# Kernel tuning notes

Hardware: AMD Instinct MI355X
Metric: run time of the kernel (lower is better)

The kernel has to match this reference:

```python
import jax, jax.numpy as jnp
import numpy as np

B, H, W, DIM = 4, 128, 128, 64
HEADS, DH, DR = 8, 64, 16
INNER = HEADS * DH  # 512
HID3 = 3 * DR       # 48, wavelet-MLP in_channels
HIDX = 2 * HID3     # 96, wavelet-MLP hidden


def _conv(x, w, stride=1, pad=0, groups=1):
    return jax.lax.conv_general_dilated(
        x, w, (stride, stride), [(pad, pad), (pad, pad)],
        dimension_numbers=('NCHW', 'OIHW', 'NCHW'), feature_group_count=groups)


def _gelu(x):
    return jax.nn.gelu(x, approximate=False)  # torch nn.GELU default (erf)


def _haar_kernel(C):
    h = np.array([[1., 1.], [1., 1.]]) / 2.
    g = np.array([[1., -1.], [1., -1.]]) / 2.
    ht = np.array([[1., 1.], [-1., -1.]]) / 2.
    gt = np.array([[1., -1.], [-1., 1.]]) / 2.
    k = np.stack([h, g, ht, gt])[:, None]          # [4,1,2,2]
    return jnp.asarray(np.tile(k, (C, 1, 1, 1)), jnp.float32)  # [4C,1,2,2], torch repeat layout


def _l2norm(x):
    return x / jnp.maximum(jnp.linalg.norm(x, axis=-1, keepdims=True), 1e-12)


def _spatial(x, dw, pw, gamma):  # SpitialUnit, x NHWC
    t = x.transpose(0, 3, 1, 2)
    C = t.shape[1]
    y = _conv(t, dw, pad=1, groups=C)
    y = _conv(_gelu(y), pw)
    return (t + gamma * y).transpose(0, 2, 3, 1)


def _fourier(x, al_pw, al_dw, ah_pw, ah_dw, ph_pw, ph_scale):  # FourierUnit, x NHWC
    t = x.transpose(0, 3, 1, 2)
    Bc, C, Hc, Wc = t.shape
    X = jnp.fft.rfft2(t, norm='ortho')
    amp, phase = jnp.abs(X), jnp.angle(X)
    Hf, Wf = amp.shape[-2], amp.shape[-1]
    yy = jnp.linspace(0., 1., Hf)[:, None]
    xx = jnp.linspace(0., 1., Wf)[None, :]
    rr = jnp.sqrt(yy ** 2 + xx ** 2)
    low = jax.nn.sigmoid((0.25 - rr) * 20.0)
    high = 1.0 - low
    a_lo = _conv(_gelu(_conv(amp * low[None, None], al_pw)), al_dw, pad=1, groups=C)
    a_hi = _conv(_gelu(_conv(amp * high[None, None], ah_pw)), ah_dw, pad=1, groups=C)
    amp_out = a_lo + a_hi
    phase_out = phase + ph_scale * _conv(phase, ph_pw)
    Y = jax.lax.complex(amp_out * jnp.cos(phase_out), amp_out * jnp.sin(phase_out))
    out = jnp.fft.irfft2(Y, s=(Hc, Wc), norm='ortho')
    return out.transpose(0, 2, 3, 1)


def _wavelet(x, bn_gamma, bn_beta, mlp_in, mlp_dw, mlp_out, res_scale):  # WaveletUnit, x NHWC (H,W even)
    t = x.transpose(0, 3, 1, 2)
    Bc, C, Hc, Wc = t.shape
    y = _conv(t, _haar_kernel(C), stride=2, groups=C)           # [B,4C,H/2,W/2]
    LL, LH, HL, HH = jnp.split(y, 4, axis=1)                    # torch chunk layout
    high = jnp.concatenate([LH, HL, HH], axis=1)                # [B,3C,H/2,W/2]
    # BatchNorm2d in eval mode: running_mean=0, running_var=1, eps=1e-5
    n = high * (bn_gamma / jnp.sqrt(1.0 + 1e-5))[None, :, None, None] + bn_beta[None, :, None, None]
    m = _conv(n, mlp_in)
    m = _gelu(_conv(m, mlp_dw, pad=1, groups=m.shape[1]))
    m = _conv(m, mlp_out)
    high_enh = high + res_scale * m
    x1, x2, x3 = jnp.split(high_enh, 3, axis=1)
    # IWT: out[..., 2i+p, 2j+q] = [LL, x1; x2, x3][p,q]
    arr = jnp.stack([jnp.stack([LL, x1], -1), jnp.stack([x2, x3], -1)], axis=-2)  # [B,C,h,w,p,q]
    Hh, Wh = LL.shape[-2], LL.shape[-1]
    out = arr.transpose(0, 1, 2, 4, 3, 5).reshape(Bc, C, Hh * 2, Wh * 2)
    return out.transpose(0, 2, 3, 1)


def reference(x_in, Wq, Wk, Wv, Wr, We, qs_dw, qs_pw, qs_gamma,
              al_pw, al_dw, ah_pw, ah_dw, ph_pw, ph_scale,
              bn_gamma, bn_beta, mlp_in, mlp_dw, mlp_out, res_scale,
              rescale, Wproj, bproj):
    b, h, w, c = x_in.shape
    hw = h * w
    heads = rescale.shape[0]
    dh = Wq.shape[1] // heads
    dr = Wr.shape[1]
    x = x_in.reshape(b, hw, c)
    q_inp, k_inp, v_inp = x @ Wq, x @ Wk, x @ Wv
    q_dim = (q_inp @ Wr).reshape(b, h, w, dr)
    k_dim = (k_inp @ Wr).reshape(b, h, w, dr)
    v_dim = (v_inp @ Wr).reshape(b, h, w, dr)
    q_mix = _spatial(q_dim, qs_dw, qs_pw, qs_gamma)
    k_mix = _fourier(k_dim, al_pw, al_dw, ah_pw, ah_dw, ph_pw, ph_scale)
    v_mix = _wavelet(v_dim, bn_gamma, bn_beta, mlp_in, mlp_dw, mlp_out, res_scale)
    q_new = q_mix.reshape(b, hw, dr) @ We
    k_new = k_mix.reshape(b, hw, dr) @ We
    v_new = v_mix.reshape(b, hw, dr) @ We

    def pack(t):  # -> [b, heads, dh, hw]
        return t.reshape(b, hw, heads, dh).transpose(0, 2, 3, 1)

    q, k, v = pack(q_new), pack(k_new), pack(v_new)
    q, k = _l2norm(q), _l2norm(k)                       # normalize over hw
    attn = jnp.einsum('bhdn,bhen->bhde', k, q)          # channel attention [b,H,dh,dh]
    attn = jax.nn.softmax(attn * rescale[None], axis=-1)
    o = jnp.einsum('bhde,bhen->bhdn', attn, v)          # [b,H,dh,hw]
    o = o.transpose(0, 3, 1, 2).reshape(b, hw, heads * dh)
    return (o @ Wproj + bproj).reshape(b, h, w, c)


def setup_inputs() -> dict:
    key = jax.random.key(0)
    ks = jax.random.split(key, 20)

    def nrm(k, shape, s=0.02):
        return jax.random.normal(k, shape, jnp.float32) * s

    return {
        'x_in': jax.random.normal(ks[0], (B, H, W, DIM), jnp.float32),
        'Wq': nrm(ks[1], (DIM, INNER)), 'Wk': nrm(ks[2], (DIM, INNER)), 'Wv': nrm(ks[3], (DIM, INNER)),
        'Wr': nrm(ks[4], (INNER, DR)), 'We': nrm(ks[5], (DR, INNER)),
        'qs_dw': nrm(ks[6], (DR, 1, 3, 3)), 'qs_pw': nrm(ks[7], (DR, DR, 1, 1)),
        'qs_gamma': jnp.zeros((1, DR, 1, 1), jnp.float32),
        'al_pw': nrm(ks[8], (DR, DR, 1, 1)), 'al_dw': nrm(ks[9], (DR, 1, 3, 3)),
        'ah_pw': nrm(ks[10], (DR, DR, 1, 1)), 'ah_dw': nrm(ks[11], (DR, 1, 3, 3)),
        'ph_pw': nrm(ks[12], (DR, DR, 1, 1)), 'ph_scale': jnp.asarray(0.01, jnp.float32),
        'bn_gamma': jnp.ones((HID3,), jnp.float32), 'bn_beta': jnp.zeros((HID3,), jnp.float32),
        'mlp_in': nrm(ks[13], (HIDX, HID3, 1, 1)), 'mlp_dw': nrm(ks[14], (HIDX, 1, 3, 3)),
        'mlp_out': nrm(ks[15], (HID3, HIDX, 1, 1)), 'res_scale': jnp.ones((1,), jnp.float32),
        'rescale': jnp.ones((HEADS, 1, 1), jnp.float32),
        'Wproj': nrm(ks[16], (INNER, DIM)), 'bproj': jnp.zeros((DIM,), jnp.float32),
    }
```

## Files before the change

kernel.cpp:

```cpp
#include <hip/hip_runtime.h>
#include <hip/hip_bf16.h>
#include <math.h>

#define HW 16384

__device__ __forceinline__ float LD(const void* p, long i, int bf){
  return bf ? __bfloat162float(((const __hip_bfloat16*)p)[i]) : ((const float*)p)[i];
}
__device__ __forceinline__ float geluf(float x){ return 0.5f*x*(1.0f + erff(x*0.70710678118654752f)); }
__device__ __forceinline__ int rev7(int i){ return (int)(__brev((unsigned)i)>>25); }

__device__ __forceinline__ void fft128(float* Ar, float* Ai, const float* ct, const float* st,
                                       int lane, float dir){
  #pragma unroll
  for(int len=2; len<=128; len<<=1){
    int half=len>>1;
    int pos = lane & (half-1);
    int i1 = ((lane & ~(half-1))<<1) | pos;
    int i2 = i1 + half;
    int tw = pos * (128/len);
    float wr = ct[tw], wi = dir*st[tw];
    float xr=Ar[i2], xi=Ai[i2];
    float tr = xr*wr - xi*wi;
    float ti = xr*wi + xi*wr;
    float ur=Ar[i1], ui=Ai[i1];
    Ar[i1]=ur+tr; Ai[i1]=ui+ti;
    Ar[i2]=ur-tr; Ai[i2]=ui-ti;
  }
}

#define MAKE_TWP(ct,st) { int tt=threadIdx.x; if(tt<128){ float ang=6.283185307179586f*(float)tt/128.f; float s_,c_; sincosf(ang,&s_,&c_); (ct)[tt]=c_; (st)[tt]=s_; } }

#define OFF_M    0
#define OFF_G    3072
#define OFF_MB   6144
#define OFF_FLAG 10240
#define OFF_QDIM 16384
#define OFF_KDIM (16384 + 1048576)
#define OFF_VDIM (16384 + 2*1048576)
#define OFF_QMIX (16384 + 3*1048576)
#define OFF_KMIX (16384 + 4*1048576)
#define OFF_S    (16384 + 5*1048576)
#define FSZ 532480

__global__ void k_head(const void* Wq, const void* Wk, const void* Wv,
                       const void* Wr, const void* bng, float* ws){
  __shared__ float wr[8192];
  __shared__ float part[256];
  int blk=blockIdx.x, t=threadIdx.x;
  if(blk==48){
    for(int i=3072+t;i<10240;i+=256) ws[i]=0.f;
    if(t==0){
      float v = ((const float*)bng)[0];
      ((int*)ws)[OFF_FLAG] = (v==1.0f) ? 0 : 1;
    }
    return;
  }
  int bf = (((const float*)bng)[0]==1.0f) ? 0 : 1;
  int mat=blk>>4, seg=blk&15;
  const void* Wsrc = mat==0 ? Wq : (mat==1 ? Wk : Wv);
  for(int i=t;i<8192;i+=256) wr[i]=LD(Wr,i,bf);
  __syncthreads();
  int o=t&63, jseg=t>>6;
  int c=seg*4+(o>>4), r=o&15;
  float acc=0.f;
  for(int j=jseg*128;j<jseg*128+128;j++) acc += LD(Wsrc,(long)c*512+j,bf)*wr[j*16+r];
  part[jseg*64+o]=acc;
  __syncthreads();
  if(t<64){
    float s=part[t]+part[64+t]+part[128+t]+part[192+t];
    int cc=seg*4+(t>>4), rr=t&15;
    ws[mat*1024 + cc*16 + rr]=s;
  }
}

__global__ void k_dims(const void* x, const float* ws,
                       float* qd, float* kd, float* vd, const int* flg){
  int bf=*flg;
  __shared__ float xs[16*64];
  __shared__ float ms[3*1024];
  int b = blockIdx.x>>10;
  int pix0 = (blockIdx.x & 1023)<<4;
  int t = threadIdx.x;
  for(int i=t;i<3072;i+=256) ms[i]=ws[i];
  long base = ((long)b*HW + pix0)*64;
  for(int i=t;i<1024;i+=256) xs[i]=LD(x, base+i, bf);
  __syncthreads();
  int p=t>>4, r=t&15;
  float aq=0.f,ak=0.f,av=0.f;
  for(int c=0;c<64;c++){
    float xv = xs[p*64+c];
    aq += xv*ms[c*16+r];
    ak += xv*ms[1024+c*16+r];
    av += xv*ms[2048+c*16+r];
  }
  long o = ((long)b*HW + pix0)*16 + t;
  qd[o]=aq; kd[o]=ak; vd[o]=av;
}

__global__ void k_mix3(const float* qd, float* qm, const void* dw, const void* pw, const void* gamma,
                       const float* kd, float* Rre, float* Rim,
                       const float* vd, float* m96, const void* win, const void* bng, const void* bnb,
                       const int* flg){
  __shared__ float smem[9664];
  int bf=*flg;
  int blk=blockIdx.x, t=threadIdx.x;
  if(blk<256){
    float* tile=smem; float* dws=smem+8704; float* pws=smem+8848; float* gsm=smem+9104;
    int b=blk>>6, y0=(blk&63)<<1;
    for(int i=t;i<144;i+=256) dws[i]=LD(dw,i,bf);
    if(t<256) pws[t]=LD(pw,t,bf);
    if(t<16) gsm[t]=LD(gamma,t,bf);
    for(int i=t;i<8192;i+=256){
      int ry=i>>11, rem=i&2047, xx=rem>>4, ch=rem&15;
      int yy=y0-1+ry;
      tile[(ry*128+xx)*17+ch] = (yy>=0&&yy<128) ? qd[(long)(b*128+yy)*2048 + rem] : 0.f;
    }
    __syncthreads();
    int ty=t>>7, x=t&127;
    float g[16];
    for(int ch=0;ch<16;ch++){
      float acc=0.f;
      for(int p=0;p<3;p++)
        for(int q=0;q<3;q++){
          int xx=x-1+q;
          if(xx>=0&&xx<128) acc += dws[ch*9+p*3+q]*tile[((ty+p)*128+xx)*17+ch];
        }
      g[ch]=geluf(acc);
    }
    long ob = ((long)(b*128+y0+ty)*128 + x)*16;
    for(int c=0;c<16;c++){
      float acc=0.f;
      for(int ch=0;ch<16;ch++) acc += pws[c*16+ch]*g[ch];
      qm[ob+c] = tile[((1+ty)*128+x)*17+c] + gsm[c]*acc;
    }
  } else if(blk<512){
    float* slab=smem; float* outre=smem+4160; float* outim=smem+6272;
    float* Ar=smem+8384; float* Ai=smem+8896; float* ct=smem+9408; float* st=smem+9536;
    int blk2=blk-256;
    int b=blk2>>6, y0=(blk2&63)<<1;
    MAKE_TWP(ct,st);
    long gbase = ((long)(b*128+y0))*2048;
    for(int e=t;e<4096;e+=256){
      int yl=e>>11, rem=e&2047, x=rem>>4, c=rem&15;
      slab[yl*2080 + c*130 + x] = kd[gbase + e];
    }
    __syncthreads();
    int w=t>>6, l=t&63, wb=w<<7;
    for(int li=w; li<32; li+=4){
      int yl=li>>4, c=li&15;
      int sb = yl*2080 + c*130;
      float v0=slab[sb+l], v1=slab[sb+64+l];
      int r0=rev7(l), r1=rev7(64+l);
      Ar[wb+r0]=v0; Ai[wb+r0]=0.f;
      Ar[wb+r1]=v1; Ai[wb+r1]=0.f;
      fft128(Ar+wb, Ai+wb, ct, st, l, -1.f);
      int ob = yl*1056 + c*66;
      outre[ob+l]=Ar[wb+l]; outim[ob+l]=Ai[wb+l];
      if(l==0){ outre[ob+64]=Ar[wb+64]; outim[ob+64]=Ai[wb+64]; }
    }
    __syncthreads();
    long obase = ((long)(b*128+y0))*1040;
    for(int e=t;e<2080;e+=256){
      int yl=e/1040, rem=e%1040, v=rem>>4, c=rem&15;
      Rre[obase+e]=outre[yl*1056 + c*66 + v];
      Rim[obase+e]=outim[yl*1056 + c*66 + v];
    }
  } else {
    float* wi=smem; float* vds=smem+4608; float* ns=smem+5632;
    float* gsm=smem+6400; float* bsm=smem+6448;
    int blk3=blk-512;
    int b = blk3>>8;
    int ij0 = (blk3&255)<<4;
    for(int i=t;i<4608;i+=256){ int cc=i/96, ch=i%96; wi[cc*96+ch]=LD(win,(long)ch*48+cc,bf); }
    if(t<48){ gsm[t]=LD(bng,t,bf)*(1.f/sqrtf(1.f+1e-5f)); bsm[t]=LD(bnb,t,bf); }
    int i0 = ij0>>6, j0 = ij0&63;
    long rb0 = ((long)(b*128 + 2*i0)*128 + 2*j0)*16;
    for(int i=t;i<512;i+=256){ vds[i]=vd[rb0+i]; vds[512+i]=vd[rb0+2048+i]; }
    __syncthreads();
    for(int o=t;o<768;o+=256){
      int p=o/48, cc2=o%48;
      int m=cc2+16, c=m>>2, f=m&3;
      float a =vds[(2*p)*16+c],     bv=vds[(2*p+1)*16+c];
      float cv=vds[512+(2*p)*16+c], dv=vds[512+(2*p+1)*16+c];
      float v;
      if(f==0)      v=(a+bv+cv+dv);
      else if(f==1) v=(a-bv+cv-dv);
      else if(f==2) v=(a+bv-cv-dv);
      else          v=(a-bv-cv+dv);
      ns[o] = v*0.5f*gsm[cc2]+bsm[cc2];
    }
    __syncthreads();
    long ob = ((long)b*4096 + ij0)*96;
    for(int o=t;o<1536;o+=256){
      int p=o/96, ch=o%96;
      float acc=0.f;
      for(int cc=0;cc<48;cc++) acc += wi[cc*96+ch]*ns[p*48+cc];
      m96[ob+o]=acc;
    }
  }
}

__global__ void k_fft_col(const float* Rre, const float* Rim,
                          float* glo, float* ghi, float* pho,
                          const void* alpw, const void* ahpw,
                          const void* phpw, const void* phs, const int* flg){
  __shared__ float sre[2080], sim[2080];
  __shared__ float og[2080], oh[2080], op[2080];
  __shared__ float Ar[512], Ai[512];
  __shared__ float ct[128], st[128];
  __shared__ float wl[256], wh[256], wp[256];
  int t=threadIdx.x;
  int bf=*flg;
  int b = blockIdx.x/65, v = blockIdx.x%65;
  MAKE_TWP(ct,st);
  wl[t]=LD(alpw,t,bf); wh[t]=LD(ahpw,t,bf); wp[t]=LD(phpw,t,bf);
  long ibase = ((long)b*128)*1040 + v*16;
  for(int e=t;e<2048;e+=256){
    int y=e>>4, c=e&15;
    sre[c*130+y]=Rre[ibase + (long)y*1040 + c];
    sim[c*130+y]=Rim[ibase + (long)y*1040 + c];
  }
  __syncthreads();
  int w=t>>6, l=t&63, wb=w<<7;
  const float inv=1.f/128.f;
  for(int c=w; c<16; c+=4){
    int sb=c*130;
    float x0r=sre[sb+l], x0i=sim[sb+l], x1r=sre[sb+64+l], x1i=sim[sb+64+l];
    int r0=rev7(l), r1=rev7(64+l);
    Ar[wb+r0]=x0r; Ai[wb+r0]=x0i;
    Ar[wb+r1]=x1r; Ai[wb+r1]=x1i;
    fft128(Ar+wb, Ai+wb, ct, st, l, -1.f);
    float re0=Ar[wb+l]*inv, im0=Ai[wb+l]*inv;
    float re1=Ar[wb+64+l]*inv, im1=Ai[wb+64+l]*inv;
    sre[sb+l]=sqrtf(re0*re0+im0*im0); sim[sb+l]=atan2f(im0,re0);
    sre[sb+64+l]=sqrtf(re1*re1+im1*im1); sim[sb+64+l]=atan2f(im1,re1);
  }
  __syncthreads();
  {
    int u = t&127, half = t>>7;
    float yy=(float)u/127.f, xx=(float)v/64.f;
    float rr=sqrtf(yy*yy+xx*xx);
    float lo = 1.f/(1.f+expf((rr-0.25f)*20.f));
    float hi = 1.f-lo;
    float av[16], pv[16];
    for(int ch=0;ch<16;ch++){ av[ch]=sre[ch*130+u]; pv[ch]=sim[ch*130+u]; }
    float pscale = LD(phs,0,bf);
    for(int c=half*8;c<half*8+8;c++){
      float al=0.f, ah=0.f, pp=0.f;
      for(int ch=0;ch<16;ch++){
        float a=av[ch];
        al += wl[c*16+ch]*(a*lo);
        ah += wh[c*16+ch]*(a*hi);
        pp += wp[c*16+ch]*pv[ch];
      }
      og[c*130+u]=geluf(al); oh[c*130+u]=geluf(ah); op[c*130+u]=pv[c]+pscale*pp;
    }
  }
  __syncthreads();
  long obase = ((long)b*128)*1040 + v*16;
  for(int e=t;e<2048;e+=256){
    int u=e>>4, c=e&15;
    long o = obase + (long)u*1040 + c;
    glo[o]=og[c*130+u]; ghi[o]=oh[c*130+u]; pho[o]=op[c*130+u];
  }
}

__global__ void k_four_dw(const float* glo, const float* ghi, const float* pho,
                          float* Yre, float* Yim,
                          const void* aldw, const void* ahdw, const int* flg){
  int bf=*flg;
  __shared__ float wl[144], wh[144];
  int t=threadIdx.x;
  if(t<144){wl[t]=LD(aldw,t,bf); wh[t]=LD(ahdw,t,bf);}
  __syncthreads();
  long o = (long)blockIdx.x*256+t;
  int c=(int)(o&15); long r=o>>4; int v=(int)(r%65); long r2=r/65; int u=(int)(r2&127); int b=(int)(r2>>7);
  float acc=0.f;
  for(int dp=0;dp<3;dp++){
    int uu=u-1+dp; if(uu<0||uu>=128) continue;
    for(int dq=0;dq<3;dq++){
      int vv=v-1+dq; if(vv<0||vv>=65) continue;
      long idx=(((long)(b*128+uu))*65+vv)*16+c;
      acc += wl[c*9+dp*3+dq]*glo[idx] + wh[c*9+dp*3+dq]*ghi[idx];
    }
  }
  float pvv = pho[o];
  float s_,c_; sincosf(pvv,&s_,&c_);
  Yre[o]=acc*c_; Yim[o]=acc*s_;
}

__global__ void k_ifft_col(const float* Yre, const float* Yim, float* Zre, float* Zim){
  __shared__ float sre[2080], sim[2080];
  __shared__ float Ar[512], Ai[512];
  __shared__ float ct[128], st[128];
  int t=threadIdx.x;
  int b = blockIdx.x/65, v = blockIdx.x%65;
  MAKE_TWP(ct,st);
  long ibase = ((long)b*128)*1040 + v*16;
  for(int e=t;e<2048;e+=256){
    int u=e>>4, c=e&15;
    sre[c*130+u]=Yre[ibase + (long)u*1040 + c];
    sim[c*130+u]=Yim[ibase + (long)u*1040 + c];
  }
  __syncthreads();
  int w=t>>6, l=t&63, wb=w<<7;
  for(int c=w; c<16; c+=4){
    int sb=c*130;
    float x0r=sre[sb+l], x0i=sim[sb+l], x1r=sre[sb+64+l], x1i=sim[sb+64+l];
    int r0=rev7(l), r1=rev7(64+l);
    Ar[wb+r0]=x0r; Ai[wb+r0]=x0i;
    Ar[wb+r1]=x1r; Ai[wb+r1]=x1i;
    fft128(Ar+wb, Ai+wb, ct, st, l, +1.f);
    sre[sb+l]=Ar[wb+l]; sim[sb+l]=Ai[wb+l];
    sre[sb+64+l]=Ar[wb+64+l]; sim[sb+64+l]=Ai[wb+64+l];
  }
  __syncthreads();
  for(int e=t;e<2048;e+=256){
    int y=e>>4, c=e&15;
    Zre[ibase + (long)y*1040 + c]=sre[c*130+y];
    Zim[ibase + (long)y*1040 + c]=sim[c*130+y];
  }
}

__global__ void k_mix2(const float* Zre, const float* Zim, float* km,
                       const float* m96, float* g96, const void* wdw_, const int* flg){
  __shared__ float smem[9664];
  int blk=blockIdx.x, t=threadIdx.x;
  if(blk<256){
    float* szre=smem; float* szim=smem+2112; float* oslab=smem+4224;
    float* Ar=smem+8384; float* Ai=smem+8896; float* ct=smem+9408; float* st=smem+9536;
    int b = blk>>6, y0 = (blk&63)<<1;
    MAKE_TWP(ct,st);
    long ibase = ((long)(b*128+y0))*1040;
    for(int e=t;e<2080;e+=256){
      int yl=e/1040, rem=e%1040, v=rem>>4, c=rem&15;
      szre[yl*1056 + c*66 + v]=Zre[ibase+e];
      szim[yl*1056 + c*66 + v]=Zim[ibase+e];
    }
    __syncthreads();
    int w=t>>6, l=t&63, wb=w<<7;
    const float inv=1.f/128.f;
    for(int li=w; li<32; li+=4){
      int yl=li>>4, c=li&15;
      int sb = yl*1056 + c*66;
      float zr0 = szre[sb+l];
      float zi0 = (l==0)?0.f:szim[sb+l];
      float zr1, zi1;
      if(l==0){ zr1=szre[sb+64]; zi1=0.f; }
      else    { zr1=szre[sb+64-l]; zi1=-szim[sb+64-l]; }
      int r0=rev7(l), r1=rev7(64+l);
      Ar[wb+r0]=zr0; Ai[wb+r0]=zi0;
      Ar[wb+r1]=zr1; Ai[wb+r1]=zi1;
      fft128(Ar+wb, Ai+wb, ct, st, l, +1.f);
      int ob = yl*2080 + c*130;
      oslab[ob+l]=Ar[wb+l]*inv;
      oslab[ob+64+l]=Ar[wb+64+l]*inv;
    }
    __syncthreads();
    long obase = ((long)(b*128+y0))*2048;
    for(int e=t;e<4096;e+=256){
      int yl=e>>11, rem=e&2047, x=rem>>4, c=rem&15;
      km[obase+e]=oslab[yl*2080 + c*130 + x];
    }
  } else {
    int bf=*flg;
    float* wdw=smem;
    for(int i=t;i<864;i+=256) wdw[i]=LD(wdw_,i,bf);
    __syncthreads();
    int o = (blk-256)*256+t;
    int ch = o%96; int r = o/96; int px = r&4095; int b = r>>12;
    int i = px>>6, j = px&63;
    long mb = (long)b*393216;
    float acc=0.f;
    for(int dp=0;dp<3;dp++){ int ii=i-1+dp; if(ii<0||ii>=64) continue;
      for(int dq=0;dq<3;dq++){ int jj=j-1+dq; if(jj<0||jj>=64) continue;
        acc += wdw[ch*9+dp*3+dq]*m96[mb + (long)(ii*64+jj)*96 + ch]; } }
    g96[o]=geluf(acc);
  }
}

__global__ void k_gram(const float* qm, const float* km, float* G){
  __shared__ float qs[256*16], ks[256*16];
  int b=blockIdx.x>>5; int chunk=blockIdx.x&31;
  int t=threadIdx.x; int r=t>>4, s=t&15;
  float akq=0.f, akk=0.f, aqq=0.f;
  for(int tile=0;tile<2;tile++){
    long pb=((long)b*HW + chunk*512 + tile*256)*16;
    for(int i=t;i<4096;i+=256){ qs[i]=qm[pb+i]; ks[i]=km[pb+i]; }
    __syncthreads();
    for(int p=0;p<256;p++){
      float kv=ks[p*16+r], qv=qs[p*16+s];
      akq += kv*qv;
      akk += kv*ks[p*16+s];
      aqq += qs[p*16+r]*qv;
    }
    __syncthreads();
  }
  float* Gb=G + b*768;
  atomicAdd(&Gb[t], akq);
  atomicAdd(&Gb[256+t], akk);
  atomicAdd(&Gb[512+t], aqq);
}

__global__ void k_attn(const float* G, float* Mb, const void* We,
                       const void* Wproj, const void* resc, const int* flg){
  int bf=*flg;
  __shared__ float wes[16*64];
  __shared__ float gkq[256], gkk[256], gqq[256];
  __shared__ float ukq[64*16], ukk[64*16], uqq[64*16];
  __shared__ float nk[64], nq[64];
  __shared__ float A[64*64];
  __shared__ float T[64*16];
  __shared__ float wpj[64*64];
  int b=blockIdx.x>>3, h=blockIdx.x&7;
  int t=threadIdx.x;
  for(int i=t;i<1024;i+=256){ int rr=i>>6, e=i&63; wes[rr*64+e]=LD(We, (long)rr*512 + h*64 + e, bf); }
  gkq[t]=G[b*768+t]; gkk[t]=G[b*768+256+t]; gqq[t]=G[b*768+512+t];
  for(int i=t;i<4096;i+=256){ int d=i>>6, c=i&63; wpj[i]=LD(Wproj,(long)(h*64+d)*64+c,bf); }
  __syncthreads();
  for(int i=t;i<1024;i+=256){
    int d=i>>4, s=i&15;
    float a1=0.f,a2=0.f,a3=0.f;
    for(int rr=0;rr<16;rr++){ float wv=wes[rr*64+d]; a1+=wv*gkq[rr*16+s]; a2+=wv*gkk[rr*16+s]; a3+=wv*gqq[rr*16+s]; }
    ukq[i]=a1; ukk[i]=a2; uqq[i]=a3;
  }
  __syncthreads();
  if(t<64){ float a=0.f; for(int s=0;s<16;s++) a+=ukk[t*16+s]*wes[s*64+t]; nk[t]=fmaxf(sqrtf(a),1e-12f); }
  else if(t<128){ int e=t-64; float a=0.f; for(int s=0;s<16;s++) a+=uqq[e*16+s]*wes[s*64+e]; nq[e]=fmaxf(sqrtf(a),1e-12f); }
  __syncthreads();
  float rsc=LD(resc,h,bf);
  for(int i=t;i<4096;i+=256){
    int d=i>>6, e=i&63;
    float a=0.f; for(int s=0;s<16;s++) a+=ukq[d*16+s]*wes[s*64+e];
    A[i]=a/(nk[d]*nq[e])*rsc;
  }
  __syncthreads();
  if(t<64){
    int d=t; float m=-1e30f;
    for(int e=0;e<64;e++) m=fmaxf(m,A[d*64+e]);
    float sum=0.f;
    for(int e=0;e<64;e++){ float ev=expf(A[d*64+e]-m); A[d*64+e]=ev; sum+=ev; }
    float inv=1.f/sum;
    for(int e=0;e<64;e++) A[d*64+e]*=inv;
  }
  __syncthreads();
  for(int i=t;i<1024;i+=256){
    int d=i>>4, s=i&15;
    float a=0.f; for(int e=0;e<64;e++) a+=A[d*64+e]*wes[s*64+e];
    T[i]=a;
  }
  __syncthreads();
  for(int i=t;i<1024;i+=256){
    int s=i>>6, c=i&63;
    float a=0.f; for(int d=0;d<64;d++) a+=T[d*16+s]*wpj[d*64+c];
    atomicAdd(&Mb[b*1024 + s*64 + c], a);
  }
}

__global__ void k_epi2(const float* g96, const float* vd, const float* Mb_,
                       const void* wout_, const void* rs_, const void* bproj,
                       void* out, const int* flg){
  int bf=*flg;
  __shared__ __align__(16) float sg[32*104];
  __shared__ __align__(16) float swt[48*100];
  __shared__ __align__(16) float smb[1024];
  __shared__ float sbias[64];
  int t=threadIdx.x;
  int b = blockIdx.x>>7;
  int rem = blockIdx.x&127;
  int gi = rem>>1;
  int gj0 = (rem&1)<<5;

  long gb = ((long)b*4096 + gi*64 + gj0)*96;
  for(int e=t;e<3072;e+=256){ int px=e/96, ch=e-px*96; sg[px*104+ch]=g96[gb+e]; }
  for(int e=t;e<4608;e+=256){ int cc=e/96, ch=e-cc*96; swt[cc*100+ch]=LD(wout_, e, bf); }
  for(int i=t;i<1024;i+=256) smb[i]=Mb_[b*1024+i];
  if(t<64) sbias[t]=LD(bproj,t,bf);
  __syncthreads();

  int tpx=t>>4, tcc=t&15;
  int px0=tpx<<1, cc0=tcc*3;
  float a00=0.f,a01=0.f,a02=0.f,a10=0.f,a11=0.f,a12=0.f;
  const float4* g4=(const float4*)sg;
  const float4* w4=(const float4*)swt;
  #pragma unroll 4
  for(int ch4=0; ch4<24; ch4++){
    float4 ga=g4[px0*26+ch4], gbv=g4[(px0+1)*26+ch4];
    float4 w0=w4[cc0*25+ch4], w1=w4[(cc0+1)*25+ch4], w2=w4[(cc0+2)*25+ch4];
    a00 += ga.x*w0.x+ga.y*w0.y+ga.z*w0.z+ga.w*w0.w;
    a01 += ga.x*w1.x+ga.y*w1.y+ga.z*w1.z+ga.w*w1.w;
    a02 += ga.x*w2.x+ga.y*w2.y+ga.z*w2.z+ga.w*w2.w;
    a10 += gbv.x*w0.x+gbv.y*w0.y+gbv.z*w0.z+gbv.w*w0.w;
    a11 += gbv.x*w1.x+gbv.y*w1.y+gbv.z*w1.z+gbv.w*w1.w;
    a12 += gbv.x*w2.x+gbv.y*w2.y+gbv.z*w2.z+gbv.w*w2.w;
  }
  __syncthreads();

  float* she = sg;
  float rs=LD(rs_,0,bf);
  float accv[2][3]={{a00,a01,a02},{a10,a11,a12}};
  #pragma unroll
  for(int i=0;i<2;i++)
    #pragma unroll
    for(int j=0;j<3;j++){
      int pxl=px0+i, cc=cc0+j, gj=gj0+pxl;
      int m=cc+16, c=m>>2, f=m&3;
      long vb=((long)(b*128+2*gi)*128 + 2*gj)*16;
      float a=vd[vb+c], bv=vd[vb+16+c], cv=vd[vb+2048+c], dv=vd[vb+2064+c];
      float hv;
      if(f==0)      hv=(a+bv+cv+dv);
      else if(f==1) hv=(a-bv+cv-dv);
      else if(f==2) hv=(a+bv-cv-dv);
      else          hv=(a-bv-cv+dv);
      she[pxl*64 + 16 + cc] = hv*0.5f + rs*accv[i][j];
    }
  for(int o=t;o<512;o+=256){
    int pxl=o>>4, c16=o&15, gj=gj0+pxl;
    int c=c16>>2, f=c16&3;
    long vb=((long)(b*128+2*gi)*128 + 2*gj)*16;
    float a=vd[vb+c], bv=vd[vb+16+c], cv=vd[vb+2048+c], dv=vd[vb+2064+c];
    float hv;
    if(f==0)      hv=(a+bv+cv+dv);
    else if(f==1) hv=(a-bv+cv-dv);
    else if(f==2) hv=(a+bv-cv-dv);
    else          hv=(a-bv-cv+dv);
    she[pxl*64 + c16] = hv*0.5f;
  }
  __syncthreads();

  int c=t&63, xg=t>>6;
  float mbr[16];
  #pragma unroll
  for(int s=0;s<16;s++) mbr[s]=smb[s*64+c];
  float bb=sbias[c];
  long ob0 = ((long)(b*128+2*gi)*128 + 2*gj0)*64;
  for(int k=0;k<32;k++){
    int o=xg+(k<<2);
    int r=o>>6, xl=o&63;
    int hp=xl>>1, pos=((r&1)<<1)|(xl&1);
    const float4* h4=(const float4*)(she + hp*64 + pos*16);
    float4 h0=h4[0],h1=h4[1],h2=h4[2],h3=h4[3];
    float acc=bb;
    acc += h0.x*mbr[0]+h0.y*mbr[1]+h0.z*mbr[2]+h0.w*mbr[3];
    acc += h1.x*mbr[4]+h1.y*mbr[5]+h1.z*mbr[6]+h1.w*mbr[7];
    acc += h2.x*mbr[8]+h2.y*mbr[9]+h2.z*mbr[10]+h2.w*mbr[11];
    acc += h3.x*mbr[12]+h3.y*mbr[13]+h3.z*mbr[14]+h3.w*mbr[15];
    long oo = ob0 + (long)r*8192 + (long)xl*64 + c;
    if(bf) ((__hip_bfloat16*)out)[oo]=__float2bfloat16(acc);
    else   ((float*)out)[oo]=acc;
  }
}

extern "C" void kernel_launch(void* const* d_in, const int* in_sizes, int n_in,
                              void* d_out, int out_size, void* d_ws, size_t ws_size,
                              hipStream_t stream) {
  const void* x_in   = d_in[0];
  const void* Wq     = d_in[1];
  const void* Wk     = d_in[2];
  const void* Wv     = d_in[3];
  const void* Wr     = d_in[4];
  const void* We     = d_in[5];
  const void* qs_dw  = d_in[6];
  const void* qs_pw  = d_in[7];
  const void* qs_g   = d_in[8];
  const void* al_pw  = d_in[9];
  const void* al_dw  = d_in[10];
  const void* ah_pw  = d_in[11];
  const void* ah_dw  = d_in[12];
  const void* ph_pw  = d_in[13];
  const void* ph_s   = d_in[14];
  const void* bn_g   = d_in[15];
  const void* bn_b   = d_in[16];
  const void* mlp_in = d_in[17];
  const void* mlp_dw = d_in[18];
  const void* mlp_out= d_in[19];
  const void* res_s  = d_in[20];
  const void* rescale= d_in[21];
  const void* Wproj  = d_in[22];
  const void* bproj  = d_in[23];
  float* ws = (float*)d_ws;
  const int* flg = ((const int*)ws) + OFF_FLAG;

  float* FA = ws + OFF_S;
  float* FB = FA + FSZ;
  float* FC = FB + FSZ;
  float* FD = FC + FSZ;
  float* FE = FD + FSZ;
  float* M96 = FE + FSZ;
  float* G96 = ws + OFF_QDIM;

  k_head<<<49,256,0,stream>>>(Wq,Wk,Wv,Wr,bn_g, ws);
  k_dims<<<4096,256,0,stream>>>(x_in, ws, ws+OFF_QDIM, ws+OFF_KDIM, ws+OFF_VDIM, flg);
  k_mix3<<<1536,256,0,stream>>>(ws+OFF_QDIM, ws+OFF_QMIX, qs_dw, qs_pw, qs_g,
                                ws+OFF_KDIM, FA, FB,
                                ws+OFF_VDIM, M96, mlp_in, bn_g, bn_b, flg);
  k_fft_col<<<260,256,0,stream>>>(FA, FB, FC, FD, FE, al_pw, ah_pw, ph_pw, ph_s, flg);
  k_four_dw<<<2080,256,0,stream>>>(FC, FD, FE, FA, FB, al_dw, ah_dw, flg);
  k_ifft_col<<<260,256,0,stream>>>(FA, FB, FC, FD);
  k_mix2<<<6400,256,0,stream>>>(FC, FD, ws+OFF_KMIX, M96, G96, mlp_dw, flg);
  k_gram<<<128,256,0,stream>>>(ws+OFF_QMIX, ws+OFF_KMIX, ws+OFF_G);
  k_attn<<<32,256,0,stream>>>(ws+OFF_G, ws+OFF_MB, We, Wproj, rescale, flg);
  k_epi2<<<512,256,0,stream>>>(G96, ws+OFF_VDIM, ws+OFF_MB, mlp_out, res_s, bproj, d_out, flg);
}
```

Before: 295.6 us.

## Register-tile dims and wavelet-MLP projections, prepack weights, split gram blocks

```diff
diff --git a/kernel.cpp b/kernel.cpp
--- a/kernel.cpp
+++ b/kernel.cpp
@@ -35,6 +35,9 @@
 #define OFF_G    3072
 #define OFF_MB   6144
 #define OFF_FLAG 10240
+#define OFF_WIN  10752
+#define OFF_GSM  15360
+#define OFF_BSM  15408
 #define OFF_QDIM 16384
 #define OFF_KDIM (16384 + 1048576)
 #define OFF_VDIM (16384 + 2*1048576)
@@ -44,12 +47,19 @@
 #define FSZ 532480
 
 __global__ void k_head(const void* Wq, const void* Wk, const void* Wv,
-                       const void* Wr, const void* bng, float* ws){
+                       const void* Wr, const void* bng, const void* bnb,
+                       const void* mlp_in_, float* ws){
   __shared__ float wr[8192];
   __shared__ float part[256];
   int blk=blockIdx.x, t=threadIdx.x;
   if(blk==48){
+    int bf = (((const float*)bng)[0]==1.0f) ? 0 : 1;
     for(int i=3072+t;i<10240;i+=256) ws[i]=0.f;
+    for(int i=t;i<4608;i+=256) ws[OFF_WIN+i]=LD(mlp_in_, i, bf);
+    if(t<48){
+      ws[OFF_GSM+t]=LD(bng,t,bf)*(1.f/sqrtf(1.f+1e-5f));
+      ws[OFF_BSM+t]=LD(bnb,t,bf);
+    }
     if(t==0){
       float v = ((const float*)bng)[0];
       ((int*)ws)[OFF_FLAG] = (v==1.0f) ? 0 : 1;
@@ -70,39 +80,70 @@
   if(t<64){
     float s=part[t]+part[64+t]+part[128+t]+part[192+t];
     int cc=seg*4+(t>>4), rr=t&15;
-    ws[mat*1024 + cc*16 + rr]=s;
+    ws[(mat*16+rr)*64 + cc]=s;
   }
 }
 
 __global__ void k_dims(const void* x, const float* ws,
                        float* qd, float* kd, float* vd, const int* flg){
   int bf=*flg;
-  __shared__ float xs[16*64];
-  __shared__ float ms[3*1024];
-  int b = blockIdx.x>>10;
-  int pix0 = (blockIdx.x & 1023)<<4;
-  int t = threadIdx.x;
-  for(int i=t;i<3072;i+=256) ms[i]=ws[i];
-  long base = ((long)b*HW + pix0)*64;
-  for(int i=t;i<1024;i+=256) xs[i]=LD(x, base+i, bf);
-  __syncthreads();
-  int p=t>>4, r=t&15;
-  float aq=0.f,ak=0.f,av=0.f;
-  for(int c=0;c<64;c++){
-    float xv = xs[p*64+c];
-    aq += xv*ms[c*16+r];
-    ak += xv*ms[1024+c*16+r];
-    av += xv*ms[2048+c*16+r];
-  }
-  long o = ((long)b*HW + pix0)*16 + t;
-  qd[o]=aq; kd[o]=ak; vd[o]=av;
+  __shared__ float sh[128*49];
+  int t=threadIdx.x;
+  int b = blockIdx.x>>7;
+  int pix0 = (blockIdx.x&127)<<7;
+  int w=t>>6, l=t&63;
+  int pxl = ((w&1)<<6) + l;
+  int rh = w>>1;
+  long base = ((long)b*HW + pix0 + pxl)*64;
+
+  float xr[64];
+  if(!bf){
+    const float4* xp = (const float4*)((const float*)x + base);
+    #pragma unroll
+    for(int k=0;k<16;k++){
+      float4 v = xp[k];
+      xr[4*k]=v.x; xr[4*k+1]=v.y; xr[4*k+2]=v.z; xr[4*k+3]=v.w;
+    }
+  } else {
+    const uint4* xp = (const uint4*)((const __hip_bfloat16*)x + base);
+    #pragma unroll
+    for(int k=0;k<8;k++){
+      uint4 u = xp[k];
+      unsigned uu[4]={u.x,u.y,u.z,u.w};
+      #pragma unroll
+      for(int q=0;q<4;q++){
+        xr[8*k+2*q]   = __uint_as_float((uu[q]&0xffffu)<<16);
+        xr[8*k+2*q+1] = __uint_as_float(uu[q]&0xffff0000u);
+      }
+    }
+  }
+  for(int r=rh*24; r<rh*24+24; r++){
+    const float* mrow = ws + r*64;
+    float a0=0.f,a1=0.f,a2=0.f,a3=0.f;
+    #pragma unroll
+    for(int c=0;c<64;c+=4){
+      a0 += xr[c]  *mrow[c];
+      a1 += xr[c+1]*mrow[c+1];
+      a2 += xr[c+2]*mrow[c+2];
+      a3 += xr[c+3]*mrow[c+3];
+    }
+    sh[pxl*49 + r] = (a0+a1)+(a2+a3);
+  }
+  __syncthreads();
+  long ob = ((long)b*HW + pix0)*16;
+  for(int e=t;e<2048;e+=256){
+    int px=e>>4, rr=e&15;
+    qd[ob+e]=sh[px*49 + rr];
+    kd[ob+e]=sh[px*49 + 16 + rr];
+    vd[ob+e]=sh[px*49 + 32 + rr];
+  }
 }
 
 __global__ void k_mix3(const float* qd, float* qm, const void* dw, const void* pw, const void* gamma,
                        const float* kd, float* Rre, float* Rim,
-                       const float* vd, float* m96, const void* win, const void* bng, const void* bnb,
+                       const float* vd, float* m96, const float* wsb,
                        const int* flg){
-  __shared__ float smem[9664];
+  __shared__ float smem[12416];
   int bf=*flg;
   int blk=blockIdx.x, t=threadIdx.x;
   if(blk<256){
@@ -167,36 +208,61 @@
       Rim[obase+e]=outim[yl*1056 + c*66 + v];
     }
   } else {
-    float* wi=smem; float* vds=smem+4608; float* ns=smem+5632;
-    float* gsm=smem+6400; float* bsm=smem+6448;
-    int blk3=blk-512;
-    int b = blk3>>8;
-    int ij0 = (blk3&255)<<4;
-    for(int i=t;i<4608;i+=256){ int cc=i/96, ch=i%96; wi[cc*96+ch]=LD(win,(long)ch*48+cc,bf); }
-    if(t<48){ gsm[t]=LD(bng,t,bf)*(1.f/sqrtf(1.f+1e-5f)); bsm[t]=LD(bnb,t,bf); }
-    int i0 = ij0>>6, j0 = ij0&63;
-    long rb0 = ((long)(b*128 + 2*i0)*128 + 2*j0)*16;
-    for(int i=t;i<512;i+=256){ vds[i]=vd[rb0+i]; vds[512+i]=vd[rb0+2048+i]; }
+    float* sm=smem;
+    const float* winf = wsb + OFF_WIN;
+    const float* gsmf = wsb + OFF_GSM;
+    const float* bsmf = wsb + OFF_BSM;
+    int idx3 = blk-512;
+    int b = idx3>>5;
+    int hpbase = (idx3&31)<<7;
+    int w=t>>6, l=t&63;
+    int hpl = ((w>>1)<<6) + l;
+    int chh = w&1;
+    int hp = hpbase + hpl;
+    int i = hp>>6, j = hp&63;
+    float va[4][12];
+    #pragma unroll
+    for(int pi=0;pi<2;pi++)
+      #pragma unroll
+      for(int pj=0;pj<2;pj++){
+        long vb = ((long)(b*128 + 2*i+pi)*128 + (2*j+pj))*16 + 4;
+        const float4* vp=(const float4*)(vd+vb);
+        float4 v0=vp[0], v1=vp[1], v2=vp[2];
+        float* d=va[pi*2+pj];
+        d[0]=v0.x;d[1]=v0.y;d[2]=v0.z;d[3]=v0.w;
+        d[4]=v1.x;d[5]=v1.y;d[6]=v1.z;d[7]=v1.w;
+        d[8]=v2.x;d[9]=v2.y;d[10]=v2.z;d[11]=v2.w;
+      }
+    float ns[48];
+    #pragma unroll
+    for(int cc=0;cc<48;cc++){
+      int m=cc+16, c=(m>>2)-4, f=m&3;
+      float a=va[0][c], bv=va[1][c], cv=va[2][c], dvv=va[3][c];
+      float v;
+      if(f==0)      v=(a+bv+cv+dvv);
+      else if(f==1) v=(a-bv+cv-dvv);
+      else if(f==2) v=(a+bv-cv-dvv);
+      else          v=(a-bv-cv+dvv);
+      ns[cc]=v*0.5f*gsmf[cc]+bsmf[cc];
+    }
+    for(int k=0;k<48;k++){
+      int ch = chh*48 + k;
+      const float* wrow = winf + ch*48;
+      float a0=0.f,a1=0.f,a2=0.f,a3=0.f;
+      #pragma unroll
+      for(int cc=0;cc<48;cc+=4){
+        a0 += ns[cc]  *wrow[cc];
+        a1 += ns[cc+1]*wrow[cc+1];
+        a2 += ns[cc+2]*wrow[cc+2];
+        a3 += ns[cc+3]*wrow[cc+3];
+      }
+      sm[ch*129 + hpl] = (a0+a1)+(a2+a3);
+    }
     __syncthreads();
-    for(int o=t;o<768;o+=256){
-      int p=o/48, cc2=o%48;
-      int m=cc2+16, c=m>>2, f=m&3;
-      float a =vds[(2*p)*16+c],     bv=vds[(2*p+1)*16+c];
-      float cv=vds[512+(2*p)*16+c], dv=vds[512+(2*p+1)*16+c];
-      float v;
-      if(f==0)      v=(a+bv+cv+dv);
-      else if(f==1) v=(a-bv+cv-dv);
-      else if(f==2) v=(a+bv-cv-dv);
-      else          v=(a-bv-cv+dv);
-      ns[o] = v*0.5f*gsm[cc2]+bsm[cc2];
-    }
-    __syncthreads();
-    long ob = ((long)b*4096 + ij0)*96;
-    for(int o=t;o<1536;o+=256){
-      int p=o/96, ch=o%96;
-      float acc=0.f;
-      for(int cc=0;cc<48;cc++) acc += wi[cc*96+ch]*ns[p*48+cc];
-      m96[ob+o]=acc;
+    long ob = ((long)b*4096 + hpbase)*96;
+    for(int e=t;e<12288;e+=256){
+      int hpp=e/96, ch=e-hpp*96;
+      m96[ob+e]=sm[ch*129 + hpp];
     }
   }
 }
@@ -382,20 +448,17 @@
 
 __global__ void k_gram(const float* qm, const float* km, float* G){
   __shared__ float qs[256*16], ks[256*16];
-  int b=blockIdx.x>>5; int chunk=blockIdx.x&31;
+  int b=blockIdx.x>>6; int chunk=blockIdx.x&63;
   int t=threadIdx.x; int r=t>>4, s=t&15;
+  long pb=((long)b*HW + chunk*256)*16;
+  for(int i=t;i<4096;i+=256){ qs[i]=qm[pb+i]; ks[i]=km[pb+i]; }
+  __syncthreads();
   float akq=0.f, akk=0.f, aqq=0.f;
-  for(int tile=0;tile<2;tile++){
-    long pb=((long)b*HW + chunk*512 + tile*256)*16;
-    for(int i=t;i<4096;i+=256){ qs[i]=qm[pb+i]; ks[i]=km[pb+i]; }
-    __syncthreads();
-    for(int p=0;p<256;p++){
-      float kv=ks[p*16+r], qv=qs[p*16+s];
-      akq += kv*qv;
-      akk += kv*ks[p*16+s];
-      aqq += qs[p*16+r]*qv;
-    }
-    __syncthreads();
+  for(int p=0;p<256;p++){
+    float kv=ks[p*16+r], qv=qs[p*16+s];
+    akq += kv*qv;
+    akk += kv*ks[p*16+s];
+    aqq += qs[p*16+r]*qv;
   }
   float* Gb=G + b*768;
   atomicAdd(&Gb[t], akq);
@@ -590,16 +653,16 @@
   float* M96 = FE + FSZ;
   float* G96 = ws + OFF_QDIM;
 
-  k_head<<<49,256,0,stream>>>(Wq,Wk,Wv,Wr,bn_g, ws);
-  k_dims<<<4096,256,0,stream>>>(x_in, ws, ws+OFF_QDIM, ws+OFF_KDIM, ws+OFF_VDIM, flg);
-  k_mix3<<<1536,256,0,stream>>>(ws+OFF_QDIM, ws+OFF_QMIX, qs_dw, qs_pw, qs_g,
-                                ws+OFF_KDIM, FA, FB,
-                                ws+OFF_VDIM, M96, mlp_in, bn_g, bn_b, flg);
+  k_head<<<49,256,0,stream>>>(Wq,Wk,Wv,Wr,bn_g,bn_b,mlp_in, ws);
+  k_dims<<<512,256,0,stream>>>(x_in, ws, ws+OFF_QDIM, ws+OFF_KDIM, ws+OFF_VDIM, flg);
+  k_mix3<<<640,256,0,stream>>>(ws+OFF_QDIM, ws+OFF_QMIX, qs_dw, qs_pw, qs_g,
+                               ws+OFF_KDIM, FA, FB,
+                               ws+OFF_VDIM, M96, ws, flg);
   k_fft_col<<<260,256,0,stream>>>(FA, FB, FC, FD, FE, al_pw, ah_pw, ph_pw, ph_s, flg);
   k_four_dw<<<2080,256,0,stream>>>(FC, FD, FE, FA, FB, al_dw, ah_dw, flg);
   k_ifft_col<<<260,256,0,stream>>>(FA, FB, FC, FD);
   k_mix2<<<6400,256,0,stream>>>(FC, FD, ws+OFF_KMIX, M96, G96, mlp_dw, flg);
-  k_gram<<<128,256,0,stream>>>(ws+OFF_QMIX, ws+OFF_KMIX, ws+OFF_G);
+  k_gram<<<256,256,0,stream>>>(ws+OFF_QMIX, ws+OFF_KMIX, ws+OFF_G);
   k_attn<<<32,256,0,stream>>>(ws+OFF_G, ws+OFF_MB, We, Wproj, rescale, flg);
   k_epi2<<<512,256,0,stream>>>(G96, ws+OFF_VDIM, ws+OFF_MB, mlp_out, res_s, bproj, d_out, flg);
 }
```

New measurement: 383.7 us. 29.8% more time.

## Register-tile the dims projection and double gram grid parallelism

Applied to the files above, without the earlier changes.

```diff
diff --git a/kernel.cpp b/kernel.cpp
--- a/kernel.cpp
+++ b/kernel.cpp
@@ -70,32 +70,74 @@
   if(t<64){
     float s=part[t]+part[64+t]+part[128+t]+part[192+t];
     int cc=seg*4+(t>>4), rr=t&15;
-    ws[mat*1024 + cc*16 + rr]=s;
+    ws[cc*48 + mat*16 + rr]=s;
   }
 }
 
 __global__ void k_dims(const void* x, const float* ws,
                        float* qd, float* kd, float* vd, const int* flg){
   int bf=*flg;
-  __shared__ float xs[16*64];
-  __shared__ float ms[3*1024];
-  int b = blockIdx.x>>10;
-  int pix0 = (blockIdx.x & 1023)<<4;
-  int t = threadIdx.x;
+  __shared__ __align__(16) float ms[3072];
+  __shared__ __align__(16) float xs[64*130];
+  int t=threadIdx.x;
+  int b = blockIdx.x>>7;
+  int pix0 = (blockIdx.x&127)<<7;
   for(int i=t;i<3072;i+=256) ms[i]=ws[i];
   long base = ((long)b*HW + pix0)*64;
-  for(int i=t;i<1024;i+=256) xs[i]=LD(x, base+i, bf);
-  __syncthreads();
-  int p=t>>4, r=t&15;
-  float aq=0.f,ak=0.f,av=0.f;
+  if(!bf){
+    const float4* xp = (const float4*)((const float*)x + base);
+    for(int e=t;e<2048;e+=256){
+      int px=e>>4, c4=(e&15)<<2;
+      float4 v = xp[e];
+      xs[(c4  )*130+px]=v.x; xs[(c4+1)*130+px]=v.y;
+      xs[(c4+2)*130+px]=v.z; xs[(c4+3)*130+px]=v.w;
+    }
+  } else {
+    const uint4* xp = (const uint4*)((const __hip_bfloat16*)x + base);
+    for(int e=t;e<1024;e+=256){
+      int px=e>>3, c8=(e&7)<<3;
+      uint4 u = xp[e];
+      unsigned uu[4]={u.x,u.y,u.z,u.w};
+      #pragma unroll
+      for(int q=0;q<4;q++){
+        xs[(c8+2*q  )*130+px] = __uint_as_float((uu[q]&0xffffu)<<16);
+        xs[(c8+2*q+1)*130+px] = __uint_as_float(uu[q]&0xffff0000u);
+      }
+    }
+  }
+  __syncthreads();
+  int pxg=t>>2, rg=t&3;
+  int px0=pxg<<1, r0=rg*12;
+  float acc0[12], acc1[12];
+  #pragma unroll
+  for(int j=0;j<12;j++){ acc0[j]=0.f; acc1[j]=0.f; }
+  #pragma unroll 4
   for(int c=0;c<64;c++){
-    float xv = xs[p*64+c];
-    aq += xv*ms[c*16+r];
-    ak += xv*ms[1024+c*16+r];
-    av += xv*ms[2048+c*16+r];
-  }
-  long o = ((long)b*HW + pix0)*16 + t;
-  qd[o]=aq; kd[o]=ak; vd[o]=av;
+    float2 xv = *(const float2*)&xs[c*130+px0];
+    const float4* mp = (const float4*)&ms[c*48+r0];
+    float4 m0=mp[0], m1=mp[1], m2=mp[2];
+    acc0[0]+=xv.x*m0.x; acc0[1]+=xv.x*m0.y; acc0[2]+=xv.x*m0.z; acc0[3]+=xv.x*m0.w;
+    acc0[4]+=xv.x*m1.x; acc0[5]+=xv.x*m1.y; acc0[6]+=xv.x*m1.z; acc0[7]+=xv.x*m1.w;
+    acc0[8]+=xv.x*m2.x; acc0[9]+=xv.x*m2.y; acc0[10]+=xv.x*m2.z; acc0[11]+=xv.x*m2.w;
+    acc1[0]+=xv.y*m0.x; acc1[1]+=xv.y*m0.y; acc1[2]+=xv.y*m0.z; acc1[3]+=xv.y*m0.w;
+    acc1[4]+=xv.y*m1.x; acc1[5]+=xv.y*m1.y; acc1[6]+=xv.y*m1.z; acc1[7]+=xv.y*m1.w;
+    acc1[8]+=xv.y*m2.x; acc1[9]+=xv.y*m2.y; acc1[10]+=xv.y*m2.z; acc1[11]+=xv.y*m2.w;
+  }
+  __syncthreads();
+  float* sh = xs;
+  #pragma unroll
+  for(int j=0;j<12;j++){
+    sh[(px0  )*49 + r0+j] = acc0[j];
+    sh[(px0+1)*49 + r0+j] = acc1[j];
+  }
+  __syncthreads();
+  long ob = ((long)b*HW + pix0)*16;
+  for(int e=t;e<2048;e+=256){
+    int px=e>>4, rr=e&15;
+    qd[ob+e]=sh[px*49 + rr];
+    kd[ob+e]=sh[px*49 + 16 + rr];
+    vd[ob+e]=sh[px*49 + 32 + rr];
+  }
 }
 
 __global__ void k_mix3(const float* qd, float* qm, const void* dw, const void* pw, const void* gamma,
@@ -382,20 +424,17 @@
 
 __global__ void k_gram(const float* qm, const float* km, float* G){
   __shared__ float qs[256*16], ks[256*16];
-  int b=blockIdx.x>>5; int chunk=blockIdx.x&31;
+  int b=blockIdx.x>>6; int chunk=blockIdx.x&63;
   int t=threadIdx.x; int r=t>>4, s=t&15;
+  long pb=((long)b*HW + chunk*256)*16;
+  for(int i=t;i<4096;i+=256){ qs[i]=qm[pb+i]; ks[i]=km[pb+i]; }
+  __syncthreads();
   float akq=0.f, akk=0.f, aqq=0.f;
-  for(int tile=0;tile<2;tile++){
-    long pb=((long)b*HW + chunk*512 + tile*256)*16;
-    for(int i=t;i<4096;i+=256){ qs[i]=qm[pb+i]; ks[i]=km[pb+i]; }
-    __syncthreads();
-    for(int p=0;p<256;p++){
-      float kv=ks[p*16+r], qv=qs[p*16+s];
-      akq += kv*qv;
-      akk += kv*ks[p*16+s];
-      aqq += qs[p*16+r]*qv;
-    }
-    __syncthreads();
+  for(int p=0;p<256;p++){
+    float kv=ks[p*16+r], qv=qs[p*16+s];
+    akq += kv*qv;
+    akk += kv*ks[p*16+s];
+    aqq += qs[p*16+r]*qv;
   }
   float* Gb=G + b*768;
   atomicAdd(&Gb[t], akq);
@@ -591,7 +630,7 @@
   float* G96 = ws + OFF_QDIM;
 
   k_head<<<49,256,0,stream>>>(Wq,Wk,Wv,Wr,bn_g, ws);
-  k_dims<<<4096,256,0,stream>>>(x_in, ws, ws+OFF_QDIM, ws+OFF_KDIM, ws+OFF_VDIM, flg);
+  k_dims<<<512,256,0,stream>>>(x_in, ws, ws+OFF_QDIM, ws+OFF_KDIM, ws+OFF_VDIM, flg);
   k_mix3<<<1536,256,0,stream>>>(ws+OFF_QDIM, ws+OFF_QMIX, qs_dw, qs_pw, qs_g,
                                 ws+OFF_KDIM, FA, FB,
                                 ws+OFF_VDIM, M96, mlp_in, bn_g, bn_b, flg);
@@ -599,7 +638,7 @@
   k_four_dw<<<2080,256,0,stream>>>(FC, FD, FE, FA, FB, al_dw, ah_dw, flg);
   k_ifft_col<<<260,256,0,stream>>>(FA, FB, FC, FD);
   k_mix2<<<6400,256,0,stream>>>(FC, FD, ws+OFF_KMIX, M96, G96, mlp_dw, flg);
-  k_gram<<<128,256,0,stream>>>(ws+OFF_QMIX, ws+OFF_KMIX, ws+OFF_G);
+  k_gram<<<256,256,0,stream>>>(ws+OFF_QMIX, ws+OFF_KMIX, ws+OFF_G);
   k_attn<<<32,256,0,stream>>>(ws+OFF_G, ws+OFF_MB, We, Wproj, rescale, flg);
   k_epi2<<<512,256,0,stream>>>(G96, ws+OFF_VDIM, ws+OFF_MB, mlp_out, res_s, bproj, d_out, flg);
 }
```

Measured after the change: 282.8 us. -4.4%, faster.
